# Optimization experiments

Measured on AMD Instinct MI355X. Metric: run time of the kernel, lower is better.

## Reference

```python
import jax, jax.numpy as jnp
import numpy as np

N = 100000          # nodes
E = 1600000         # edges (before self loops)
F_IN = 128          # num_features
HID = 16            # hidden_channels (per head)
HEADS = 4
NCLS = 16           # num_classes (per head)
NEG_SLOPE = 0.2     # PyG GATv2Conv default


def gatv2_conv(x, src, dst, w_l, w_r, att, bias, heads, out_ch):
    """PyG GATv2Conv (concat=True, add_self_loops handled by caller).
    x: [N, Fin]; src/dst: [E']; w_l/w_r: [Fin, heads*out_ch]; att: [heads, out_ch].
    """
    n = x.shape[0]
    x_l = (x @ w_l).reshape(n, heads, out_ch)  # source-side transform
    x_r = (x @ w_r).reshape(n, heads, out_ch)  # target-side transform
    # per-edge attention logits: a^T LeakyReLU(x_l[j] + x_r[i])
    e = jax.nn.leaky_relu(x_l[src] + x_r[dst], NEG_SLOPE)   # [E', H, C]
    logits = jnp.einsum('ehc,hc->eh', e, att)               # [E', H]
    # segment softmax over incoming edges of each dst node
    m = jax.ops.segment_max(logits, dst, num_segments=n)    # [N, H]
    a = jnp.exp(logits - m[dst])
    denom = jax.ops.segment_sum(a, dst, num_segments=n)     # [N, H]
    alpha = a / denom[dst]                                  # self loops => denom > 0
    out = jax.ops.segment_sum(alpha[:, :, None] * x_l[src], dst, num_segments=n)
    return out.reshape(n, heads * out_ch) + bias


def setup_inputs() -> dict:
    key = jax.random.key(0)
    ks = jax.random.split(key, 10)
    x = jax.random.normal(ks[0], (N, F_IN), dtype=jnp.float32)
    edge_index = jax.random.randint(ks[1], (2, E), 0, N, dtype=jnp.int64)
    d1 = HEADS * HID   # 64
    s1 = 1.0 / np.sqrt(F_IN)
    s2 = 1.0 / np.sqrt(d1)
    return {
        'x': x,
        'edge_index': edge_index,
        'w_l1': jax.random.normal(ks[2], (F_IN, d1), dtype=jnp.float32) * s1,
        'w_r1': jax.random.normal(ks[3], (F_IN, d1), dtype=jnp.float32) * s1,
        'att1': jax.random.normal(ks[4], (HEADS, HID), dtype=jnp.float32) * s2,
        'b1': jnp.zeros((d1,), dtype=jnp.float32),
        'w_l2': jax.random.normal(ks[5], (d1, HEADS * NCLS), dtype=jnp.float32) * s2,
        'w_r2': jax.random.normal(ks[6], (d1, HEADS * NCLS), dtype=jnp.float32) * s2,
        'att2': jax.random.normal(ks[7], (HEADS, NCLS), dtype=jnp.float32) * (1.0 / np.sqrt(NCLS)),
        'b2': jnp.zeros((HEADS * NCLS,), dtype=jnp.float32),
    }


def reference(x, edge_index, w_l1, w_r1, att1, b1, w_l2, w_r2, att2, b2):
    # add self loops (PyG GATv2Conv default add_self_loops=True)
    loop = jnp.arange(N, dtype=edge_index.dtype)
    src = jnp.concatenate([edge_index[0], loop])
    dst = jnp.concatenate([edge_index[1], loop])
    h = gatv2_conv(x, src, dst, w_l1, w_r1, att1, b1, HEADS, HID)
    h = jax.nn.relu(h)
    out = gatv2_conv(h, src, dst, w_l2, w_r2, att2, b2, HEADS, NCLS)
    return out
```

## Files before the change

kernel.cpp:

```cpp
#include <hip/hip_runtime.h>
#include <hip/hip_fp16.h>

#define FIN 128
#define BSH 9
#define BMASK ((1 << BSH) - 1)
#define CHUNK 8192
#define BCAP 10240

typedef _Float16 half4 __attribute__((ext_vector_type(4)));
typedef _Float16 h2v __attribute__((ext_vector_type(2)));
typedef float f32x4 __attribute__((ext_vector_type(4)));

static __device__ __forceinline__ float xor1_add(float p) {
  const int sw = __builtin_amdgcn_mov_dpp(__builtin_bit_cast(int, p), 0xB1,
                                          0xF, 0xF, true);
  return p + __builtin_bit_cast(float, sw);
}

template<int K, bool FP32IN>
__global__ __launch_bounds__(256) void gemm_mfma(
    const void* __restrict__ xin, const float* __restrict__ wl,
    const float* __restrict__ wr, __half* __restrict__ outl,
    __half* __restrict__ outr, int n) {
  constexpr int WSTR = K + 4;
  __shared__ _Float16 Wt[128 * WSTR];
  const int tid = threadIdx.x;
  for (int i4 = tid; i4 < K * 16; i4 += 256) {
    const int k = i4 >> 4, c0 = (i4 & 15) << 2;
    const float4 vl = *(const float4*)&wl[k * 64 + c0];
    const float4 vr = *(const float4*)&wr[k * 64 + c0];
    Wt[(c0 + 0) * WSTR + k] = (_Float16)vl.x;
    Wt[(c0 + 1) * WSTR + k] = (_Float16)vl.y;
    Wt[(c0 + 2) * WSTR + k] = (_Float16)vl.z;
    Wt[(c0 + 3) * WSTR + k] = (_Float16)vl.w;
    Wt[(c0 + 64) * WSTR + k] = (_Float16)vr.x;
    Wt[(c0 + 65) * WSTR + k] = (_Float16)vr.y;
    Wt[(c0 + 66) * WSTR + k] = (_Float16)vr.z;
    Wt[(c0 + 67) * WSTR + k] = (_Float16)vr.w;
  }
  __syncthreads();
  const int lane = tid & 63;
  const int wv = tid >> 6;
  const int r0 = blockIdx.x * 64 + wv * 16;
  const int rowc = min(r0 + (lane & 15), n - 1);
  const int kgrp = (lane >> 4) << 2;
  const int col16 = lane & 15;
  f32x4 acc[8];
#pragma unroll
  for (int cf = 0; cf < 8; ++cf) acc[cf] = {0.f, 0.f, 0.f, 0.f};

  for (int ks = 0; ks < K / 16; ++ks) {
    const int kb = ks * 16 + kgrp;
    half4 a;
    if (FP32IN) {
      const float4 av =
          *(const float4*)((const float*)xin + (size_t)rowc * K + kb);
      a = {(_Float16)av.x, (_Float16)av.y, (_Float16)av.z, (_Float16)av.w};
    } else {
      a = *(const half4*)((const __half*)xin + (size_t)rowc * K + kb);
    }
#pragma unroll
    for (int cf = 0; cf < 8; ++cf) {
      const half4 b = *(const half4*)&Wt[(cf * 16 + col16) * WSTR + kb];
      acc[cf] = __builtin_amdgcn_mfma_f32_16x16x16f16(a, b, acc[cf], 0, 0, 0);
    }
  }
  const int crow0 = r0 + ((lane >> 4) << 2);
#pragma unroll
  for (int cf = 0; cf < 8; ++cf) {
    const int c = cf * 16 + col16;
    __half* outp = (c < 64) ? outl : outr;
    const int cc = c & 63;
#pragma unroll
    for (int r = 0; r < 4; ++r) {
      const int rr = crow0 + r;
      if (rr < n) outp[(size_t)rr * 64 + cc] = (__half)acc[cf][r];
    }
  }
}

__global__ void init_misc(int NB, int* __restrict__ gcursor,
                          const float* __restrict__ att1,
                          const float* __restrict__ att2,
                          __half* __restrict__ att1h,
                          __half* __restrict__ att2h) {
  const int t = threadIdx.x;
  if (t < NB) gcursor[t] = t * BCAP;
  if (t < 64) {
    att1h[t] = (__half)(att1[t] * 1.44269504f);
    att2h[t] = (__half)(att2[t] * 1.44269504f);
  }
}

__global__ __launch_bounds__(256) void binpass(
    const int* __restrict__ src, const int* __restrict__ dst, int E, int ET,
    int NB, int* __restrict__ gcursor, unsigned* __restrict__ sorted_val) {
  __shared__ unsigned lval[CHUNK];
  __shared__ unsigned short lrank[CHUNK];
  __shared__ unsigned char lb[CHUNK];
  __shared__ int c1[256], base[256];
  const int tid = threadIdx.x;
  c1[tid] = 0;
  __syncthreads();
  const int e0 = blockIdx.x * CHUNK;
#pragma unroll
  for (int j = 0; j < CHUNK / 256; ++j) {
    const int idx = tid + 256 * j;
    const int e = e0 + idx;
    if (e < ET) {
      int s, d;
      if (e < E) {
        s = src[e];
        d = dst[e];
      } else {
        s = d = e - E;
      }
      const int b = d >> BSH;
      lval[idx] = (unsigned)s | ((unsigned)(d & BMASK) << 17);
      lb[idx] = (unsigned char)b;
      lrank[idx] = (unsigned short)atomicAdd(&c1[b], 1);
    } else {
      lb[idx] = 255;
    }
  }
  __syncthreads();
  if (tid < NB && c1[tid] > 0) base[tid] = atomicAdd(&gcursor[tid], c1[tid]);
  __syncthreads();
#pragma unroll
  for (int j = 0; j < CHUNK / 256; ++j) {
    const int idx = tid + 256 * j;
    const int b = lb[idx];
    if (b != 255) sorted_val[base[b] + lrank[idx]] = lval[idx];
  }
}

__global__ __launch_bounds__(256) void bucket_scatter(
    const int* __restrict__ gcursor, const unsigned* __restrict__ sorted_val,
    int n, int* __restrict__ ssrc, int* __restrict__ off_beg,
    int* __restrict__ off_end) {
  __shared__ int cnt[512], sa[512], sb[512], cur[512];
  __shared__ int buf[BCAP];
  const int b = blockIdx.x;
  const int tid = threadIdx.x;
  const int node0 = b << BSH;
  const int nn = min(512, n - node0);
  const int rbase = b * BCAP;
  const int rlen = gcursor[b] - rbase;
  for (int j = tid; j < 512; j += 256) cnt[j] = 0;
  __syncthreads();
  for (int i = tid; i < rlen; i += 256)
    atomicAdd(&cnt[sorted_val[rbase + i] >> 17], 1);
  __syncthreads();
  for (int j = tid; j < 512; j += 256) sa[j] = cnt[j];
  __syncthreads();
  int* pin = sa;
  int* pout = sb;
  for (int off = 1; off < 512; off <<= 1) {
    for (int j = tid; j < 512; j += 256)
      pout[j] = pin[j] + (j >= off ? pin[j - off] : 0);
    __syncthreads();
    int* t = pin;
    pin = pout;
    pout = t;
  }
  for (int j = tid; j < 512; j += 256) {
    const int excl = pin[j] - cnt[j];
    cur[j] = excl;
    if (j < nn) {
      off_beg[node0 + j] = rbase + excl;
      off_end[node0 + j] = rbase + pin[j];
    }
  }
  __syncthreads();
  if (rlen <= BCAP) {
    for (int i = tid; i < rlen; i += 256) {
      const unsigned v = sorted_val[rbase + i];
      const int p = atomicAdd(&cur[v >> 17], 1);
      buf[p] = (int)(v & 0x1FFFFu);
    }
    __syncthreads();
    for (int i = tid; i < rlen; i += 256) ssrc[rbase + i] = buf[i];
  } else {
    for (int i = tid; i < rlen; i += 256) {
      const unsigned v = sorted_val[rbase + i];
      const int p = atomicAdd(&cur[v >> 17], 1);
      ssrc[rbase + p] = (int)(v & 0x1FFFFu);
    }
  }
}

template<bool RELU, typename OT>
__global__ __launch_bounds__(256) void node_pass(
    const int* __restrict__ off_beg, const int* __restrict__ off_end,
    const int* __restrict__ ssrc, const __half* __restrict__ xl,
    const __half* __restrict__ xr, const __half* __restrict__ atth,
    const float* __restrict__ bias, OT* __restrict__ out, int n) {
  __shared__ float part[4][8][64];
  const int lane = threadIdx.x & 63;
  const int wv = threadIdx.x >> 6;
  const int grp = lane >> 3;
  const int sl = lane & 7;
  const int d = (blockIdx.x * blockDim.x + threadIdx.x) >> 6;
  if (d >= n) return;
  const int beg = off_beg[d], end = off_end[d];
  const int deg = end - beg;

  union H8 { float4 f4; h2v h2[4]; uint4 u4; };
  H8 ath;
  ath.u4 = *(const uint4*)&atth[8 * sl];
  H8 xrv;
  xrv.f4 = *(const float4*)&xr[(size_t)d * 64 + 8 * sl];

  float acc[8] = {0.f, 0.f, 0.f, 0.f, 0.f, 0.f, 0.f, 0.f};
  float den = 0.f;

  const __half* xlp = xl + 8 * sl;
  const int sv = ssrc[min(beg + lane, end - 1)];

#define EDGE_CORE(vreg_)                                                     \
  {                                                                          \
    H8 ul;                                                                   \
    ul.f4 = (vreg_);                                                         \
    float p = 0.f;                                                           \
    _Pragma("unroll") for (int q = 0; q < 4; ++q) {                          \
      const h2v t = ul.h2[q] + xrv.h2[q];                                    \
      const h2v lk = __builtin_elementwise_max(t, t * (_Float16)0.2f);       \
      p = __builtin_amdgcn_fdot2(lk, ath.h2[q], p, false);                   \
    }                                                                        \
    p = xor1_add(p);                                                         \
    const float a = exp2f(p);                                                \
    const _Float16 ah = (_Float16)a;                                         \
    const h2v aL = {ah, (_Float16)0.f};                                      \
    const h2v aH = {(_Float16)0.f, ah};                                      \
    _Pragma("unroll") for (int q = 0; q < 4; ++q) {                          \
      acc[2 * q] = __builtin_amdgcn_fdot2(ul.h2[q], aL, acc[2 * q], false);  \
      acc[2 * q + 1] =                                                       \
          __builtin_amdgcn_fdot2(ul.h2[q], aH, acc[2 * q + 1], false);       \
    }                                                                        \
    den += a;                                                                \
  }

  if (deg <= 40) {
#define XLF(base_, dst_)                                                     \
  {                                                                          \
    const int s_ = __shfl(sv, (base_) - beg + grp);                          \
    dst_ = *(const float4*)&xlp[(size_t)s_ * 64];                            \
  }
    float4 a0, a1, nx;
    XLF(beg, a0);
    XLF(beg + 8, a1);
    int base = beg;
#pragma unroll 2
    for (; base + 8 <= end; base += 8) {
      XLF(base + 16, nx);
      EDGE_CORE(a0);
      a0 = a1;
      a1 = nx;
    }
    if (base < end) {
      if (base + grp < end) EDGE_CORE(a0);
    }
#undef XLF
  } else {
#define XLS(base_, dst_)                                                     \
  {                                                                          \
    const int idx_ = (base_) - beg + grp;                                    \
    int s_ = __shfl(sv, idx_ & 63);                                          \
    if (idx_ >= 64) s_ = ssrc[min((base_) + grp, end - 1)];                  \
    dst_ = *(const float4*)&xlp[(size_t)s_ * 64];                            \
  }
    float4 a0, a1, nx;
    XLS(beg, a0);
    XLS(beg + 8, a1);
    for (int base = beg; base < end; base += 8) {
      XLS(base + 16, nx);
      if (base + grp < end) EDGE_CORE(a0);
      a0 = a1;
      a1 = nx;
    }
#undef XLS
  }
#undef EDGE_CORE

#pragma unroll
  for (int m = 8; m <= 32; m <<= 1) den += __shfl_xor(den, m);
  const float den_c = __shfl(den, (lane >> 4) << 1);

  *(float4*)&part[wv][grp][8 * sl] = make_float4(acc[0], acc[1], acc[2], acc[3]);
  *(float4*)&part[wv][grp][8 * sl + 4] =
      make_float4(acc[4], acc[5], acc[6], acc[7]);
  float s = 0.f;
#pragma unroll
  for (int g = 0; g < 8; ++g) s += part[wv][g][lane];

  float v = s / den_c + bias[lane];
  if (RELU) v = fmaxf(v, 0.f);
  out[(size_t)d * 64 + lane] = (OT)v;
}

extern "C" void kernel_launch(void* const* d_in, const int* in_sizes, int n_in,
                              void* d_out, int out_size, void* d_ws, size_t ws_size,
                              hipStream_t stream) {
  const float* x    = (const float*)d_in[0];
  const int*   ei   = (const int*)d_in[1];
  const float* wl1  = (const float*)d_in[2];
  const float* wr1  = (const float*)d_in[3];
  const float* att1 = (const float*)d_in[4];
  const float* b1   = (const float*)d_in[5];
  const float* wl2  = (const float*)d_in[6];
  const float* wr2  = (const float*)d_in[7];
  const float* att2 = (const float*)d_in[8];
  const float* b2   = (const float*)d_in[9];
  float* out = (float*)d_out;

  const int n = in_sizes[0] / FIN;
  const int E = in_sizes[1] / 2;
  const int ET = E + n;
  const int* src = ei;
  const int* dst = ei + E;
  const int NB = (n + (1 << BSH) - 1) >> BSH;

  __half* A  = (__half*)d_ws;
  __half* B  = A + (size_t)n * 64;
  __half* Hh = B + (size_t)n * 64;
  __half* att1h = Hh + (size_t)n * 64;
  __half* att2h = att1h + 64;
  int* off_beg = (int*)(att2h + 64);
  int* off_end = off_beg + n;
  int* gcursor = off_end + n;
  unsigned* sorted_val = (unsigned*)(gcursor + 256);
  int* ssrc = (int*)(sorted_val + (size_t)NB * BCAP);

  const int nbin = (ET + CHUNK - 1) / CHUNK;

  init_misc<<<1, 256, 0, stream>>>(NB, gcursor, att1, att2, att1h, att2h);
  binpass<<<nbin, 256, 0, stream>>>(src, dst, E, ET, NB, gcursor, sorted_val);
  bucket_scatter<<<NB, 256, 0, stream>>>(gcursor, sorted_val, n, ssrc,
                                         off_beg, off_end);

  const int gb = (n + 63) / 64;
  const int nb = (n * 64 + 255) / 256;

  gemm_mfma<128, true><<<gb, 256, 0, stream>>>(x, wl1, wr1, A, B, n);
  node_pass<true, __half><<<nb, 256, 0, stream>>>(off_beg, off_end, ssrc, A, B,
                                                  att1h, b1, Hh, n);

  gemm_mfma<64, false><<<gb, 256, 0, stream>>>(Hh, wl2, wr2, A, B, n);
  node_pass<false, float><<<nb, 256, 0, stream>>>(off_beg, off_end, ssrc, A, B,
                                                  att2h, b2, out, n);
}
```

Before: 165.4 us.

## Fuse bucket scatter with first GEMM and pack node offsets into int2

Merges the bucket-scatter kernel and the layer-1 GEMM into one launch, with separate block ranges for each role, so the independent GEMM work runs alongside the CSR build. The init kernel becomes a memset of the cursors, with bucket bases added in binpass, and the attention conversion moves into the fused kernel. Node offsets are stored as one int2 so node_pass does a single load. The fast-path degree threshold rises from 40 to 64. These changes cut launch count and overlap stages, at the cost of a larger shared-memory footprint per block and mixed block roles in one grid.

```diff
diff --git a/kernel.cpp b/kernel.cpp
--- a/kernel.cpp
+++ b/kernel.cpp
@@ -48,7 +48,6 @@
   f32x4 acc[8];
 #pragma unroll
   for (int cf = 0; cf < 8; ++cf) acc[cf] = {0.f, 0.f, 0.f, 0.f};
-
   for (int ks = 0; ks < K / 16; ++ks) {
     const int kb = ks * 16 + kgrp;
     half4 a;
@@ -76,19 +75,6 @@
       const int rr = crow0 + r;
       if (rr < n) outp[(size_t)rr * 64 + cc] = (__half)acc[cf][r];
     }
-  }
-}
-
-__global__ void init_misc(int NB, int* __restrict__ gcursor,
-                          const float* __restrict__ att1,
-                          const float* __restrict__ att2,
-                          __half* __restrict__ att1h,
-                          __half* __restrict__ att2h) {
-  const int t = threadIdx.x;
-  if (t < NB) gcursor[t] = t * BCAP;
-  if (t < 64) {
-    att1h[t] = (__half)(att1[t] * 1.44269504f);
-    att2h[t] = (__half)(att2[t] * 1.44269504f);
   }
 }
 
@@ -124,7 +110,8 @@
     }
   }
   __syncthreads();
-  if (tid < NB && c1[tid] > 0) base[tid] = atomicAdd(&gcursor[tid], c1[tid]);
+  if (tid < NB && c1[tid] > 0)
+    base[tid] = tid * BCAP + atomicAdd(&gcursor[tid], c1[tid]);
   __syncthreads();
 #pragma unroll
   for (int j = 0; j < CHUNK / 256; ++j) {
@@ -134,67 +121,130 @@
   }
 }
 
-__global__ __launch_bounds__(256) void bucket_scatter(
+__global__ __launch_bounds__(256) void scatter_gemm1(
     const int* __restrict__ gcursor, const unsigned* __restrict__ sorted_val,
-    int n, int* __restrict__ ssrc, int* __restrict__ off_beg,
-    int* __restrict__ off_end) {
-  __shared__ int cnt[512], sa[512], sb[512], cur[512];
-  __shared__ int buf[BCAP];
-  const int b = blockIdx.x;
+    int n, int* __restrict__ ssrc, int2* __restrict__ off2,
+    const float* __restrict__ x, const float* __restrict__ wl,
+    const float* __restrict__ wr, __half* __restrict__ outl,
+    __half* __restrict__ outr, int NB,
+    const float* __restrict__ att1, const float* __restrict__ att2,
+    __half* __restrict__ att1h, __half* __restrict__ att2h) {
+  __shared__ __align__(16) char smem[49152];
   const int tid = threadIdx.x;
-  const int node0 = b << BSH;
-  const int nn = min(512, n - node0);
-  const int rbase = b * BCAP;
-  const int rlen = gcursor[b] - rbase;
-  for (int j = tid; j < 512; j += 256) cnt[j] = 0;
-  __syncthreads();
-  for (int i = tid; i < rlen; i += 256)
-    atomicAdd(&cnt[sorted_val[rbase + i] >> 17], 1);
-  __syncthreads();
-  for (int j = tid; j < 512; j += 256) sa[j] = cnt[j];
-  __syncthreads();
-  int* pin = sa;
-  int* pout = sb;
-  for (int off = 1; off < 512; off <<= 1) {
-    for (int j = tid; j < 512; j += 256)
-      pout[j] = pin[j] + (j >= off ? pin[j - off] : 0);
+
+  if (blockIdx.x == 0 && tid < 64) {
+    att1h[tid] = (__half)(att1[tid] * 1.44269504f);
+    att2h[tid] = (__half)(att2[tid] * 1.44269504f);
+  }
+
+  if (blockIdx.x < (unsigned)NB) {
+    int* cnt = (int*)smem;
+    int* sa = cnt + 512;
+    int* sb = sa + 512;
+    int* cur = sb + 512;
+    int* buf = cur + 512;
+    const int b = blockIdx.x;
+    const int node0 = b << BSH;
+    const int nn = min(512, n - node0);
+    const int rbase = b * BCAP;
+    const int rlen = gcursor[b];
+    for (int j = tid; j < 512; j += 256) cnt[j] = 0;
     __syncthreads();
-    int* t = pin;
-    pin = pout;
-    pout = t;
-  }
-  for (int j = tid; j < 512; j += 256) {
-    const int excl = pin[j] - cnt[j];
-    cur[j] = excl;
-    if (j < nn) {
-      off_beg[node0 + j] = rbase + excl;
-      off_end[node0 + j] = rbase + pin[j];
-    }
-  }
-  __syncthreads();
-  if (rlen <= BCAP) {
-    for (int i = tid; i < rlen; i += 256) {
-      const unsigned v = sorted_val[rbase + i];
-      const int p = atomicAdd(&cur[v >> 17], 1);
-      buf[p] = (int)(v & 0x1FFFFu);
-    }
+    for (int i = tid; i < rlen; i += 256)
+      atomicAdd(&cnt[sorted_val[rbase + i] >> 17], 1);
     __syncthreads();
-    for (int i = tid; i < rlen; i += 256) ssrc[rbase + i] = buf[i];
+    for (int j = tid; j < 512; j += 256) sa[j] = cnt[j];
+    __syncthreads();
+    int* pin = sa;
+    int* pout = sb;
+    for (int off = 1; off < 512; off <<= 1) {
+      for (int j = tid; j < 512; j += 256)
+        pout[j] = pin[j] + (j >= off ? pin[j - off] : 0);
+      __syncthreads();
+      int* t = pin;
+      pin = pout;
+      pout = t;
+    }
+    for (int j = tid; j < 512; j += 256) {
+      const int excl = pin[j] - cnt[j];
+      cur[j] = excl;
+      if (j < nn) off2[node0 + j] = make_int2(rbase + excl, rbase + pin[j]);
+    }
+    __syncthreads();
+    if (rlen <= BCAP) {
+      for (int i = tid; i < rlen; i += 256) {
+        const unsigned v = sorted_val[rbase + i];
+        const int p = atomicAdd(&cur[v >> 17], 1);
+        buf[p] = (int)(v & 0x1FFFFu);
+      }
+      __syncthreads();
+      for (int i = tid; i < rlen; i += 256) ssrc[rbase + i] = buf[i];
+    } else {
+      for (int i = tid; i < rlen; i += 256) {
+        const unsigned v = sorted_val[rbase + i];
+        const int p = atomicAdd(&cur[v >> 17], 1);
+        ssrc[rbase + p] = (int)(v & 0x1FFFFu);
+      }
+    }
   } else {
-    for (int i = tid; i < rlen; i += 256) {
-      const unsigned v = sorted_val[rbase + i];
-      const int p = atomicAdd(&cur[v >> 17], 1);
-      ssrc[rbase + p] = (int)(v & 0x1FFFFu);
+    constexpr int K = 128;
+    constexpr int WSTR = K + 4;
+    _Float16* Wt = (_Float16*)smem;
+    for (int i4 = tid; i4 < K * 16; i4 += 256) {
+      const int k = i4 >> 4, c0 = (i4 & 15) << 2;
+      const float4 vl = *(const float4*)&wl[k * 64 + c0];
+      const float4 vr = *(const float4*)&wr[k * 64 + c0];
+      Wt[(c0 + 0) * WSTR + k] = (_Float16)vl.x;
+      Wt[(c0 + 1) * WSTR + k] = (_Float16)vl.y;
+      Wt[(c0 + 2) * WSTR + k] = (_Float16)vl.z;
+      Wt[(c0 + 3) * WSTR + k] = (_Float16)vl.w;
+      Wt[(c0 + 64) * WSTR + k] = (_Float16)vr.x;
+      Wt[(c0 + 65) * WSTR + k] = (_Float16)vr.y;
+      Wt[(c0 + 66) * WSTR + k] = (_Float16)vr.z;
+      Wt[(c0 + 67) * WSTR + k] = (_Float16)vr.w;
+    }
+    __syncthreads();
+    const int lane = tid & 63;
+    const int wv = tid >> 6;
+    const int r0 = (blockIdx.x - NB) * 64 + wv * 16;
+    const int rowc = min(r0 + (lane & 15), n - 1);
+    const int kgrp = (lane >> 4) << 2;
+    const int col16 = lane & 15;
+    f32x4 acc[8];
+#pragma unroll
+    for (int cf = 0; cf < 8; ++cf) acc[cf] = {0.f, 0.f, 0.f, 0.f};
+    for (int ks = 0; ks < K / 16; ++ks) {
+      const int kb = ks * 16 + kgrp;
+      const float4 av = *(const float4*)&x[(size_t)rowc * K + kb];
+      const half4 a = {(_Float16)av.x, (_Float16)av.y, (_Float16)av.z,
+                       (_Float16)av.w};
+#pragma unroll
+      for (int cf = 0; cf < 8; ++cf) {
+        const half4 bb = *(const half4*)&Wt[(cf * 16 + col16) * WSTR + kb];
+        acc[cf] = __builtin_amdgcn_mfma_f32_16x16x16f16(a, bb, acc[cf], 0, 0, 0);
+      }
+    }
+    const int crow0 = r0 + ((lane >> 4) << 2);
+#pragma unroll
+    for (int cf = 0; cf < 8; ++cf) {
+      const int c = cf * 16 + col16;
+      __half* outp = (c < 64) ? outl : outr;
+      const int cc = c & 63;
+#pragma unroll
+      for (int r = 0; r < 4; ++r) {
+        const int rr = crow0 + r;
+        if (rr < n) outp[(size_t)rr * 64 + cc] = (__half)acc[cf][r];
+      }
     }
   }
 }
 
 template<bool RELU, typename OT>
 __global__ __launch_bounds__(256) void node_pass(
-    const int* __restrict__ off_beg, const int* __restrict__ off_end,
-    const int* __restrict__ ssrc, const __half* __restrict__ xl,
-    const __half* __restrict__ xr, const __half* __restrict__ atth,
-    const float* __restrict__ bias, OT* __restrict__ out, int n) {
+    const int2* __restrict__ off2, const int* __restrict__ ssrc,
+    const __half* __restrict__ xl, const __half* __restrict__ xr,
+    const __half* __restrict__ atth, const float* __restrict__ bias,
+    OT* __restrict__ out, int n) {
   __shared__ float part[4][8][64];
   const int lane = threadIdx.x & 63;
   const int wv = threadIdx.x >> 6;
@@ -202,7 +252,8 @@
   const int sl = lane & 7;
   const int d = (blockIdx.x * blockDim.x + threadIdx.x) >> 6;
   if (d >= n) return;
-  const int beg = off_beg[d], end = off_end[d];
+  const int2 oo = off2[d];
+  const int beg = oo.x, end = oo.y;
   const int deg = end - beg;
 
   union H8 { float4 f4; h2v h2[4]; uint4 u4; };
@@ -240,7 +291,7 @@
     den += a;                                                                \
   }
 
-  if (deg <= 40) {
+  if (deg <= 64) {
 #define XLF(base_, dst_)                                                     \
   {                                                                          \
     const int s_ = __shfl(sv, (base_) - beg + grp);                          \
@@ -325,27 +376,25 @@
   __half* Hh = B + (size_t)n * 64;
   __half* att1h = Hh + (size_t)n * 64;
   __half* att2h = att1h + 64;
-  int* off_beg = (int*)(att2h + 64);
-  int* off_end = off_beg + n;
-  int* gcursor = off_end + n;
+  int2* off2 = (int2*)(att2h + 64);
+  int* gcursor = (int*)(off2 + n);
   unsigned* sorted_val = (unsigned*)(gcursor + 256);
   int* ssrc = (int*)(sorted_val + (size_t)NB * BCAP);
 
   const int nbin = (ET + CHUNK - 1) / CHUNK;
-
-  init_misc<<<1, 256, 0, stream>>>(NB, gcursor, att1, att2, att1h, att2h);
-  binpass<<<nbin, 256, 0, stream>>>(src, dst, E, ET, NB, gcursor, sorted_val);
-  bucket_scatter<<<NB, 256, 0, stream>>>(gcursor, sorted_val, n, ssrc,
-                                         off_beg, off_end);
-
   const int gb = (n + 63) / 64;
   const int nb = (n * 64 + 255) / 256;
 
-  gemm_mfma<128, true><<<gb, 256, 0, stream>>>(x, wl1, wr1, A, B, n);
-  node_pass<true, __half><<<nb, 256, 0, stream>>>(off_beg, off_end, ssrc, A, B,
-                                                  att1h, b1, Hh, n);
+  hipMemsetAsync(gcursor, 0, 256 * sizeof(int), stream);
+  binpass<<<nbin, 256, 0, stream>>>(src, dst, E, ET, NB, gcursor, sorted_val);
+  scatter_gemm1<<<NB + gb, 256, 0, stream>>>(
+      gcursor, sorted_val, n, ssrc, off2, x, wl1, wr1, A, B, NB, att1, att2,
+      att1h, att2h);
+
+  node_pass<true, __half><<<nb, 256, 0, stream>>>(off2, ssrc, A, B, att1h, b1,
+                                                  Hh, n);
 
   gemm_mfma<64, false><<<gb, 256, 0, stream>>>(Hh, wl2, wr2, A, B, n);
-  node_pass<false, float><<<nb, 256, 0, stream>>>(off_beg, off_end, ssrc, A, B,
-                                                  att2h, b2, out, n);
-}
+  node_pass<false, float><<<nb, 256, 0, stream>>>(off2, ssrc, A, B, att2h, b2,
+                                                  out, n);
+}
```

New measurement: 155.0 us. -6.3%, faster.
